# Performance work log

Measured on AMD Instinct MI355X. Metric: run time of the kernel, lower is better.

The kernel has to match this reference:

```python
import jax, jax.numpy as jnp
import numpy as np

N_QUBITS = 4
N_LAYERS = 2


def _apply_1q(psi, U, wire, n):
    # psi: (B, 2**n) complex; U: (2,2) or (B,2,2) complex; wire 0 = most-significant (PennyLane order)
    B = psi.shape[0]
    L, R = 2 ** wire, 2 ** (n - 1 - wire)
    psi = psi.reshape(B, L, 2, R)
    if U.ndim == 3:
        psi = jnp.einsum('bij,bljr->blir', U, psi)
    else:
        psi = jnp.einsum('ij,bljr->blir', U, psi)
    return psi.reshape(B, 2 ** n)


def _apply_cnot(psi, wire, n):
    # CNOT with control=wire, target=wire+1 (adjacent wires)
    B = psi.shape[0]
    L, R = 2 ** wire, 2 ** (n - 2 - wire)
    psi = psi.reshape(B, L, 2, 2, R)
    flipped = psi[:, :, 1, ::-1, :]  # X on target when control=1
    psi = jnp.concatenate([psi[:, :, :1], flipped[:, :, None]], axis=2)
    return psi.reshape(B, 2 ** n)


def _ry(theta):
    # theta: (B,) -> (B,2,2) complex RY matrices
    c, s = jnp.cos(theta / 2), jnp.sin(theta / 2)
    U = jnp.stack([jnp.stack([c, -s], -1), jnp.stack([s, c], -1)], -2)
    return U.astype(jnp.complex64)


def _rot(phi, theta, omega):
    # PennyLane Rot = RZ(omega) RY(theta) RZ(phi); returns (2,2) complex
    c, s = jnp.cos(theta / 2), jnp.sin(theta / 2)
    u00 = jnp.exp(-0.5j * (phi + omega)) * c
    u01 = -jnp.exp(0.5j * (phi - omega)) * s
    u10 = jnp.exp(-0.5j * (phi - omega)) * s
    u11 = jnp.exp(0.5j * (phi + omega)) * c
    return jnp.stack([jnp.stack([u00, u01]), jnp.stack([u10, u11])]).astype(jnp.complex64)


def _prepare_register(angles, W, n, n_layers):
    # angles: (B, n) already tanh'd; W: (n_layers, n, 3)
    B = angles.shape[0]
    psi = jnp.zeros((B, 2 ** n), jnp.complex64).at[:, 0].set(1.0)
    for i in range(n):
        psi = _apply_1q(psi, _ry(angles[:, i] * np.pi), i, n)
    for layer in range(n_layers):
        for i in range(n):
            psi = _apply_1q(psi, _rot(W[layer, i, 0], W[layer, i, 1], W[layer, i, 2]), i, n)
        for i in range(n - 1):
            psi = _apply_cnot(psi, i, n)
    return psi


def setup_inputs() -> dict:
    key = jax.random.key(0)
    k1, k2, k3, k4 = jax.random.split(key, 4)
    B, D = 262144, 64
    return {
        'query': jax.random.normal(k1, (B, D), dtype=jnp.float32),
        'key': jax.random.normal(k2, (B, D), dtype=jnp.float32),
        'W_q': jax.random.normal(k3, (N_LAYERS, N_QUBITS, 3), dtype=jnp.float32) * 0.1,
        'W_k': jax.random.normal(k4, (N_LAYERS, N_QUBITS, 3), dtype=jnp.float32) * 0.1,
    }


def reference(query, key, W_q, W_k):
    n = N_QUBITS
    q = jnp.tanh(query[..., :n])
    k = jnp.tanh(key[..., :n])
    psi_q = _prepare_register(q, W_q, n, N_LAYERS)  # (B, 16)
    psi_k = _prepare_register(k, W_k, n, N_LAYERS)  # (B, 16)
    # Swap test: <Z_ancilla> = |<psi_q|psi_k>|^2
    ov = jnp.sum(jnp.conj(psi_q) * psi_k, axis=-1)
    score = ov.real ** 2 + ov.imag ** 2
    return (1.0 + score) / 2.0
```

## Files before the change

kernel.cpp:

```cpp
#include <hip/hip_runtime.h>

__device__ __forceinline__ float2 cmul(float2 a, float2 b) {
    return make_float2(a.x*b.x - a.y*b.y, a.x*b.y + a.y*b.x);
}
__device__ __forceinline__ float2 cfma(float2 a, float2 b, float2 acc) {
    acc.x = fmaf(a.x, b.x, fmaf(-a.y, b.y, acc.x));
    acc.y = fmaf(a.x, b.y, fmaf( a.y, b.x, acc.y));
    return acc;
}
__device__ __forceinline__ float2 cfma_conj(float2 a, float2 b, float2 acc) {
    acc.x = fmaf(a.x, b.x, fmaf( a.y, b.y, acc.x));
    acc.y = fmaf(a.x, b.y, fmaf(-a.y, b.x, acc.y));
    return acc;
}

__global__ void qdp_setup(const float* __restrict__ Wq,
                          const float* __restrict__ Wk,
                          float2* __restrict__ G) {
    const int t = threadIdx.x;
    float2 cq[16], ck[16];
    #pragma unroll
    for (int x = 0; x < 16; ++x) {
        cq[x] = make_float2(x == t ? 1.0f : 0.0f, 0.0f);
        ck[x] = cq[x];
    }

    #pragma unroll
    for (int layer = 0; layer < 2; ++layer) {
        #pragma unroll
        for (int w = 0; w < 4; ++w) {
            const int mask = 1 << (3 - w);
            #pragma unroll
            for (int which = 0; which < 2; ++which) {
                const float* wp = (which ? Wk : Wq) + layer*12 + w*3;
                float2* col = which ? ck : cq;
                const float phi = wp[0], th = wp[1], om = wp[2];
                const float ht = 0.5f*th, ap = 0.5f*(phi+om), am = 0.5f*(phi-om);
                const float c   = __cosf(ht),  s   = __sinf(ht);
                const float cap = __cosf(ap),  sap = __sinf(ap);
                const float cam = __cosf(am),  sam = __sinf(am);
                const float2 u00 = make_float2( c*cap, -c*sap);
                const float2 u01 = make_float2(-s*cam, -s*sam);
                const float2 u10 = make_float2( s*cam, -s*sam);
                const float2 u11 = make_float2( c*cap,  c*sap);
                #pragma unroll
                for (int x = 0; x < 16; ++x) {
                    if (x & mask) continue;
                    const int y = x | mask;
                    const float2 a = col[x], b = col[y];
                    float2 nx = cmul(u00, a); nx = cfma(u01, b, nx);
                    float2 ny = cmul(u10, a); ny = cfma(u11, b, ny);
                    col[x] = nx; col[y] = ny;
                }
            }
        }
        #pragma unroll
        for (int w = 0; w < 3; ++w) {
            const int mc = 1 << (3 - w);
            const int mt = 1 << (2 - w);
            #pragma unroll
            for (int x = 0; x < 16; ++x) {
                if ((x & mc) && !(x & mt)) {
                    const int y = x | mt;
                    float2 tmp = cq[x]; cq[x] = cq[y]; cq[y] = tmp;
                    tmp = ck[x]; ck[x] = ck[y]; ck[y] = tmp;
                }
            }
        }
    }

    __shared__ float2 MqL[16][16];
    #pragma unroll
    for (int kx = 0; kx < 16; ++kx) MqL[kx][t] = cq[kx];
    __syncthreads();

    #pragma unroll
    for (int i = 0; i < 16; ++i) {
        float2 acc = make_float2(0.0f, 0.0f);
        #pragma unroll
        for (int kx = 0; kx < 16; ++kx)
            acc = cfma_conj(MqL[kx][i], ck[kx], acc);
        G[i*16 + t] = acc;
    }
}

__device__ __forceinline__ float fast_tanh(float x) {
    const float e = __expf(2.0f * x);
    return 1.0f - 2.0f / (e + 1.0f);
}

__global__ __launch_bounds__(256)
void qdp_main(const float* __restrict__ Q, const float* __restrict__ K,
              const float2* __restrict__ G, float* __restrict__ out, int B) {
    __shared__ float4 lq[256], lk[256];
    const int t = threadIdx.x;
    const long b0 = (long)blockIdx.x * 256;

    const float4* Qb = reinterpret_cast<const float4*>(Q + b0 * 64);
    const float4* Kb = reinterpret_cast<const float4*>(K + b0 * 64);

    float4 vq[8], vk[8];
    #pragma unroll
    for (int s = 0; s < 8; ++s) {
        const int f   = s * 256 + t;
        const int idx = ((f >> 3) << 4) + (f & 7);
        vq[s] = Qb[idx];
        vk[s] = Kb[idx];
    }
    #pragma unroll
    for (int s = 0; s < 8; ++s) {
        if ((t & 7) == 0) {
            const int row = (s * 256 + t) >> 3;
            lq[row] = vq[s];
            lk[row] = vk[s];
        }
    }
    __syncthreads();

    const float4 qv = lq[t];
    const float4 kv = lk[t];

    float cqa[4], sqa[4], cka[4], ska[4];
    {
        const float qa[4] = {qv.x, qv.y, qv.z, qv.w};
        const float ka[4] = {kv.x, kv.y, kv.z, kv.w};
        #pragma unroll
        for (int i = 0; i < 4; ++i) {
            const float tq = fast_tanh(qa[i]) * 1.57079632679489662f;
            const float tk = fast_tanh(ka[i]) * 1.57079632679489662f;
            __sincosf(tq, &sqa[i], &cqa[i]);
            __sincosf(tk, &ska[i], &cka[i]);
        }
    }

    const float pq01[4] = {cqa[0]*cqa[1], cqa[0]*sqa[1], sqa[0]*cqa[1], sqa[0]*sqa[1]};
    const float pq23[4] = {cqa[2]*cqa[3], cqa[2]*sqa[3], sqa[2]*cqa[3], sqa[2]*sqa[3]};
    const float pk01[4] = {cka[0]*cka[1], cka[0]*ska[1], ska[0]*cka[1], ska[0]*ska[1]};
    const float pk23[4] = {cka[2]*cka[3], cka[2]*ska[3], ska[2]*cka[3], ska[2]*ska[3]};

    float bk[16];
    #pragma unroll
    for (int j = 0; j < 16; ++j) bk[j] = pk01[j >> 2] * pk23[j & 3];

    float ovr = 0.0f, ovi = 0.0f;
    #pragma unroll
    for (int i = 0; i < 16; ++i) {
        float wr = 0.0f, wi = 0.0f;
        #pragma unroll
        for (int j = 0; j < 16; ++j) {
            const float2 g = G[i*16 + j];
            wr = fmaf(g.x, bk[j], wr);
            wi = fmaf(g.y, bk[j], wi);
        }
        const float ai = pq01[i >> 2] * pq23[i & 3];
        ovr = fmaf(ai, wr, ovr);
        ovi = fmaf(ai, wi, ovi);
    }

    out[b0 + t] = fmaf(0.5f, ovr*ovr + ovi*ovi, 0.5f);
}

extern "C" void kernel_launch(void* const* d_in, const int* in_sizes, int n_in,
                              void* d_out, int out_size, void* d_ws, size_t ws_size,
                              hipStream_t stream) {
    const float* query = (const float*)d_in[0];
    const float* key   = (const float*)d_in[1];
    const float* Wq    = (const float*)d_in[2];
    const float* Wk    = (const float*)d_in[3];
    float* out = (float*)d_out;
    float2* G  = (float2*)d_ws;

    const int B = in_sizes[0] / 64;

    qdp_setup<<<1, 16, 0, stream>>>(Wq, Wk, G);
    qdp_main<<<B / 256, 256, 0, stream>>>(query, key, G, out, B);
}
```

Before: 147.8 us.

## Fuse gate-matrix setup into main kernel and halve per-row input loads

Drops the separate single-block setup kernel. Each block now builds the 16x16 Q/K circuit matrices and their Gram product G in shared memory, using 32 threads, and reads G from LDS instead of global memory. The input load pattern also changes so each row fetches 4 float4s instead of 8, halving the bytes touched per row. In exchange, every block repeats the setup work before a barrier. That adds serial latency per block, which other resident blocks must hide.

```diff
diff --git a/kernel.cpp b/kernel.cpp
--- a/kernel.cpp
+++ b/kernel.cpp
@@ -14,103 +14,104 @@
     return acc;
 }
 
-__global__ void qdp_setup(const float* __restrict__ Wq,
-                          const float* __restrict__ Wk,
-                          float2* __restrict__ G) {
-    const int t = threadIdx.x;
-    float2 cq[16], ck[16];
-    #pragma unroll
-    for (int x = 0; x < 16; ++x) {
-        cq[x] = make_float2(x == t ? 1.0f : 0.0f, 0.0f);
-        ck[x] = cq[x];
-    }
-
-    #pragma unroll
-    for (int layer = 0; layer < 2; ++layer) {
-        #pragma unroll
-        for (int w = 0; w < 4; ++w) {
-            const int mask = 1 << (3 - w);
-            #pragma unroll
-            for (int which = 0; which < 2; ++which) {
-                const float* wp = (which ? Wk : Wq) + layer*12 + w*3;
-                float2* col = which ? ck : cq;
-                const float phi = wp[0], th = wp[1], om = wp[2];
-                const float ht = 0.5f*th, ap = 0.5f*(phi+om), am = 0.5f*(phi-om);
-                const float c   = __cosf(ht),  s   = __sinf(ht);
-                const float cap = __cosf(ap),  sap = __sinf(ap);
-                const float cam = __cosf(am),  sam = __sinf(am);
-                const float2 u00 = make_float2( c*cap, -c*sap);
-                const float2 u01 = make_float2(-s*cam, -s*sam);
-                const float2 u10 = make_float2( s*cam, -s*sam);
-                const float2 u11 = make_float2( c*cap,  c*sap);
-                #pragma unroll
-                for (int x = 0; x < 16; ++x) {
-                    if (x & mask) continue;
-                    const int y = x | mask;
-                    const float2 a = col[x], b = col[y];
-                    float2 nx = cmul(u00, a); nx = cfma(u01, b, nx);
-                    float2 ny = cmul(u10, a); ny = cfma(u11, b, ny);
-                    col[x] = nx; col[y] = ny;
-                }
-            }
-        }
-        #pragma unroll
-        for (int w = 0; w < 3; ++w) {
-            const int mc = 1 << (3 - w);
-            const int mt = 1 << (2 - w);
-            #pragma unroll
-            for (int x = 0; x < 16; ++x) {
-                if ((x & mc) && !(x & mt)) {
-                    const int y = x | mt;
-                    float2 tmp = cq[x]; cq[x] = cq[y]; cq[y] = tmp;
-                    tmp = ck[x]; ck[x] = ck[y]; ck[y] = tmp;
-                }
-            }
-        }
-    }
-
-    __shared__ float2 MqL[16][16];
-    #pragma unroll
-    for (int kx = 0; kx < 16; ++kx) MqL[kx][t] = cq[kx];
-    __syncthreads();
-
-    #pragma unroll
-    for (int i = 0; i < 16; ++i) {
-        float2 acc = make_float2(0.0f, 0.0f);
-        #pragma unroll
-        for (int kx = 0; kx < 16; ++kx)
-            acc = cfma_conj(MqL[kx][i], ck[kx], acc);
-        G[i*16 + t] = acc;
-    }
-}
-
 __device__ __forceinline__ float fast_tanh(float x) {
     const float e = __expf(2.0f * x);
     return 1.0f - 2.0f / (e + 1.0f);
 }
 
 __global__ __launch_bounds__(256)
-void qdp_main(const float* __restrict__ Q, const float* __restrict__ K,
-              const float2* __restrict__ G, float* __restrict__ out, int B) {
+void qdp_fused(const float* __restrict__ Q, const float* __restrict__ K,
+               const float* __restrict__ Wq, const float* __restrict__ Wk,
+               float* __restrict__ out) {
+    __shared__ float2 Gs[256];
+    __shared__ float2 MqL[16][16];
+    __shared__ float2 MkL[16][16];
     __shared__ float4 lq[256], lk[256];
+
     const int t = threadIdx.x;
     const long b0 = (long)blockIdx.x * 256;
-
     const float4* Qb = reinterpret_cast<const float4*>(Q + b0 * 64);
     const float4* Kb = reinterpret_cast<const float4*>(K + b0 * 64);
 
-    float4 vq[8], vk[8];
+    float4 vq[4], vk[4];
     #pragma unroll
-    for (int s = 0; s < 8; ++s) {
+    for (int s = 0; s < 4; ++s) {
         const int f   = s * 256 + t;
-        const int idx = ((f >> 3) << 4) + (f & 7);
+        const int idx = ((f >> 2) << 4) + (f & 3);
         vq[s] = Qb[idx];
         vk[s] = Kb[idx];
     }
-    #pragma unroll
-    for (int s = 0; s < 8; ++s) {
-        if ((t & 7) == 0) {
-            const int row = (s * 256 + t) >> 3;
+
+    const bool isQ = (t < 16);
+    const bool isK = (t >= 64 && t < 80);
+    if (isQ || isK) {
+        const int col  = isK ? (t - 64) : t;
+        const float* W = isK ? Wk : Wq;
+        float2 c[16];
+        #pragma unroll
+        for (int x = 0; x < 16; ++x)
+            c[x] = make_float2(x == col ? 1.0f : 0.0f, 0.0f);
+
+        #pragma unroll
+        for (int layer = 0; layer < 2; ++layer) {
+            #pragma unroll
+            for (int w = 0; w < 4; ++w) {
+                const int mask = 1 << (3 - w);
+                const float* wp = W + layer*12 + w*3;
+                const float phi = wp[0], th = wp[1], om = wp[2];
+                const float ht = 0.5f*th, ap = 0.5f*(phi+om), am = 0.5f*(phi-om);
+                const float cc  = __cosf(ht),  ss  = __sinf(ht);
+                const float cap = __cosf(ap),  sap = __sinf(ap);
+                const float cam = __cosf(am),  sam = __sinf(am);
+                const float2 u00 = make_float2( cc*cap, -cc*sap);
+                const float2 u01 = make_float2(-ss*cam, -ss*sam);
+                const float2 u10 = make_float2( ss*cam, -ss*sam);
+                const float2 u11 = make_float2( cc*cap,  cc*sap);
+                #pragma unroll
+                for (int x = 0; x < 16; ++x) {
+                    if (x & mask) continue;
+                    const int y = x | mask;
+                    const float2 a = c[x], b = c[y];
+                    float2 nx = cmul(u00, a); nx = cfma(u01, b, nx);
+                    float2 ny = cmul(u10, a); ny = cfma(u11, b, ny);
+                    c[x] = nx; c[y] = ny;
+                }
+            }
+            #pragma unroll
+            for (int w = 0; w < 3; ++w) {
+                const int mc = 1 << (3 - w);
+                const int mt = 1 << (2 - w);
+                #pragma unroll
+                for (int x = 0; x < 16; ++x) {
+                    if ((x & mc) && !(x & mt)) {
+                        const int y = x | mt;
+                        const float2 tmp = c[x]; c[x] = c[y]; c[y] = tmp;
+                    }
+                }
+            }
+        }
+        #pragma unroll
+        for (int kx = 0; kx < 16; ++kx) {
+            if (isK) MkL[kx][col] = c[kx];
+            else     MqL[kx][col] = c[kx];
+        }
+    }
+    __syncthreads();
+
+    if (t < 16) {
+        #pragma unroll
+        for (int i = 0; i < 16; ++i) {
+            float2 acc = make_float2(0.0f, 0.0f);
+            #pragma unroll
+            for (int kx = 0; kx < 16; ++kx)
+                acc = cfma_conj(MqL[kx][i], MkL[kx][t], acc);
+            Gs[i*16 + t] = acc;
+        }
+    }
+    if ((t & 3) == 0) {
+        #pragma unroll
+        for (int s = 0; s < 4; ++s) {
+            const int row = s * 64 + (t >> 2);
             lq[row] = vq[s];
             lk[row] = vk[s];
         }
@@ -148,7 +149,7 @@
         float wr = 0.0f, wi = 0.0f;
         #pragma unroll
         for (int j = 0; j < 16; ++j) {
-            const float2 g = G[i*16 + j];
+            const float2 g = Gs[i*16 + j];
             wr = fmaf(g.x, bk[j], wr);
             wi = fmaf(g.y, bk[j], wi);
         }
@@ -168,10 +169,8 @@
     const float* Wq    = (const float*)d_in[2];
     const float* Wk    = (const float*)d_in[3];
     float* out = (float*)d_out;
-    float2* G  = (float2*)d_ws;
 
     const int B = in_sizes[0] / 64;
 
-    qdp_setup<<<1, 16, 0, stream>>>(Wq, Wk, G);
-    qdp_main<<<B / 256, 256, 0, stream>>>(query, key, G, out, B);
+    qdp_fused<<<B / 256, 256, 0, stream>>>(query, key, Wq, Wk, out);
 }
```

Measured after the change: 155.3 us. +5.1%, slower.
